# Kernel optimization log

Hardware: AMD Instinct MI355X
Metric: run time of the kernel (lower is better)

The kernel has to match this reference:

```python
import jax, jax.numpy as jnp
import numpy as np

# QLSTMClassifier (quantum mode): Embedding -> QLSTM (4 quantum gate layers per step) -> Linear -> log_softmax.
# NOTE: QLSTM.forward unbinds dim 0 (batch) and cats each x:(seq,emb) with hx:(batch,hid),
# which requires batch == seq_len. We honor that with S = batch = seq_len.
S = 256   # batch == seq_len
E = 1024  # embedding_dim
H = 10    # hidden_dim == n_qubits (required by f*cx elementwise product)
V = 50257 # vocab_size
T = 50    # tagset_size


def setup_inputs() -> dict:
    key = jax.random.key(0)
    ks = jax.random.split(key, 6)
    sentence = jax.random.randint(ks[0], (S, S), 0, V)                                   # (batch, seq)
    emb_table = jax.random.normal(ks[1], (V, E), jnp.float32) * 0.02                      # nn.Embedding weight
    Wg = jax.random.normal(ks[2], (4, E + H, H), jnp.float32) * (1.0 / np.sqrt(E + H))    # forget/input/update/output linears
    bg = jnp.zeros((4, H), jnp.float32)
    theta = jax.random.normal(ks[3], (4, H), jnp.float32)                                 # trainable RX angles per gate
    W_out = jax.random.normal(ks[4], (H, T), jnp.float32) * (1.0 / np.sqrt(H))            # hidden2tag
    b_out = jnp.zeros((T,), jnp.float32)
    return dict(sentence=sentence, emb_table=emb_table, Wg=Wg, bg=bg,
                theta=theta, W_out=W_out, b_out=b_out)


def _qlayer(z, th):
    # Exact closed form of the QLayer circuit on n wires starting from |0...0>:
    #   RX(z_w) then RX(th_w) on wire w  ==> RX(a_w) with a_w = z_w + th_w (product state),
    #   then CNOT ring: CNOT(0,1), CNOT(1,2), ..., CNOT(n-2,n-1), CNOT(n-1,0),
    # Heisenberg-picture pullback of Z_w through the CNOT ring gives
    #   M_0 = Z_1 Z_2 ... Z_{n-1},   M_w = Z_0 Z_1 ... Z_w  (w >= 1),
    # and on the product state <Z_j> = cos(a_j), so expectations factorize:
    #   out_0 = prod_{j>=1} cos(a_j),  out_w = prod_{j<=w} cos(a_j).
    c = jnp.cos(z + th)                                   # (B, H)
    cum = jnp.cumprod(c, axis=-1)                         # prefix products
    tail = jnp.prod(c[:, 1:], axis=-1, keepdims=True)     # wire-0 observable
    return jnp.concatenate([tail, cum[:, 1:]], axis=-1)   # (B, H)


def reference(sentence, emb_table, Wg, bg, theta, W_out, b_out):
    embeds = emb_table[sentence]                          # (S, S, E); scan axis = dim 0 (unbind dim)
    h0 = jnp.zeros((embeds.shape[0], theta.shape[1]), embeds.dtype)

    def step(carry, x):                                   # x: (S, E)
        hx, cx = carry
        comb = jnp.concatenate([x, hx], axis=-1)          # (S, E+H)
        z = jnp.einsum('bi,gio->gbo', comb, Wg) + bg[:, None, :]  # (4, S, H)
        f = jax.nn.sigmoid(_qlayer(z[0], theta[0]))
        i = jax.nn.sigmoid(_qlayer(z[1], theta[1]))
        g = jnp.tanh(_qlayer(z[2], theta[2]))
        o = jax.nn.sigmoid(_qlayer(z[3], theta[3]))
        cx = f * cx + i * g
        hx = o * jnp.tanh(cx)
        return (hx, cx), hx

    _, outs = jax.lax.scan(step, (h0, h0), embeds)        # (S, S, H)
    logits = outs @ W_out + b_out                         # (S, S, T)
    return jax.nn.log_softmax(logits, axis=2)
```

## Files before the change

### kernel.cpp

```cpp
#include <hip/hip_runtime.h>
#include <hip/hip_bf16.h>


#define E_DIM 1024
#define H_DIM 10
#define NC 40
#define V_DIM 50257
#define EHS 10340

typedef __attribute__((ext_vector_type(8))) short bf16x8;
typedef __attribute__((ext_vector_type(4))) float f32x4;

__device__ __forceinline__ unsigned short f2bf(float f) {
    unsigned u = __float_as_uint(f);
    unsigned r = u + 0x7FFFu + ((u >> 16) & 1u);
    return (unsigned short)(r >> 16);
}

__global__ __launch_bounds__(256) void k_wt(const float* __restrict__ Wg,
                                            unsigned short* __restrict__ Bfg) {
    int i = blockIdx.x * 256 + threadIdx.x;
    if (i >= 6144) return;
    int lane = i & 63, nt = (i >> 6) % 3, c = i / 192;
    int kg = lane >> 4, n = lane & 15;
    int nc = nt * 16 + n;
    unsigned short v[8];
#pragma unroll
    for (int j = 0; j < 8; ++j) {
        int k = c * 32 + kg * 8 + j;
        float w = 0.0f;
        if (nc < NC) {
            int g = nc / H_DIM, h = nc % H_DIM;
            w = Wg[g * EHS + k * H_DIM + h];
        }
        v[j] = f2bf(w);
    }
    bf16x8* dst = (bf16x8*)(Bfg + (size_t)i * 8);
    bf16x8 pk;
#pragma unroll
    for (int j = 0; j < 8; ++j) pk[j] = (short)v[j];
    *dst = pk;
}

__global__ __launch_bounds__(256, 4) void k_gemm(const float* __restrict__ emb,
                                                 const unsigned short* __restrict__ Bfg,
                                                 float* __restrict__ zu) {
    const int tid = threadIdx.x;
    const int wave = tid >> 6, lane = tid & 63;
    const int R0 = (blockIdx.x * 4 + wave) * 16;
    const int m = lane & 15, q = lane >> 4;

    int row = R0 + m;
    if (row > V_DIM - 1) row = V_DIM - 1;
    const float* arow = emb + (size_t)row * E_DIM + q * 8;

    f32x4 acc0 = {0.f, 0.f, 0.f, 0.f}, acc1 = acc0, acc2 = acc0;

#pragma unroll 2
    for (int c = 0; c < 32; ++c) {
        f32x4 a0 = __builtin_nontemporal_load((const f32x4*)(arow + c * 32));
        f32x4 a1 = __builtin_nontemporal_load((const f32x4*)(arow + c * 32 + 4));
        bf16x8 b0 = *(const bf16x8*)(Bfg + ((size_t)(c * 3 + 0) * 64 + lane) * 8);
        bf16x8 b1 = *(const bf16x8*)(Bfg + ((size_t)(c * 3 + 1) * 64 + lane) * 8);
        bf16x8 b2 = *(const bf16x8*)(Bfg + ((size_t)(c * 3 + 2) * 64 + lane) * 8);
        bf16x8 af;
        af[0] = (short)f2bf(a0[0]); af[1] = (short)f2bf(a0[1]);
        af[2] = (short)f2bf(a0[2]); af[3] = (short)f2bf(a0[3]);
        af[4] = (short)f2bf(a1[0]); af[5] = (short)f2bf(a1[1]);
        af[6] = (short)f2bf(a1[2]); af[7] = (short)f2bf(a1[3]);
        acc0 = __builtin_amdgcn_mfma_f32_16x16x32_bf16(af, b0, acc0, 0, 0, 0);
        acc1 = __builtin_amdgcn_mfma_f32_16x16x32_bf16(af, b1, acc1, 0, 0, 0);
        acc2 = __builtin_amdgcn_mfma_f32_16x16x32_bf16(af, b2, acc2, 0, 0, 0);
    }

    const int r0 = R0 + q * 4;
#pragma unroll
    for (int i = 0; i < 4; ++i) {
        int r = r0 + i;
        if (r < V_DIM) {
            size_t o = (size_t)r * NC;
            zu[o + m] = acc0[i];
            zu[o + 16 + m] = acc1[i];
            if (m < 8) zu[o + 32 + m] = acc2[i];
        }
    }
}

template <int CTRL>
__device__ __forceinline__ float dpp1(float x) {
    return __int_as_float(__builtin_amdgcn_update_dpp(
        __float_as_int(1.0f), __float_as_int(x), CTRL, 0xF, 0xF, false));
}
#define ROW_SHR(n) (0x110 + (n))
#define ROW_SHL(n) (0x100 + (n))

__device__ __forceinline__ float rdlane(float v, int l) {
    return __int_as_float(__builtin_amdgcn_readlane(__float_as_int(v), l));
}

__global__ __launch_bounds__(128) void k_rnn(const int* __restrict__ idx,
                                             const float* __restrict__ zu,
                                             const float* __restrict__ Wg,
                                             const float* __restrict__ bg,
                                             const float* __restrict__ theta,
                                             float* __restrict__ outs) {
    __shared__ float zall[256 * NC];
    const int tid = threadIdx.x;
    const int b = blockIdx.x;

    {
        const int j = tid >> 2;
        const int qq = tid & 3;
        int tok[8];
#pragma unroll
        for (int pass = 0; pass < 8; ++pass)
            tok[pass] = idx[(size_t)(pass * 32 + j) * 256 + b];
#pragma unroll
        for (int pass = 0; pass < 8; ++pass) {
            const float* src = zu + (size_t)tok[pass] * NC + qq * 10;
            float* dst = &zall[(pass * 32 + j) * NC + qq * 10];
#pragma unroll
            for (int e = 0; e < 5; ++e)
                *(float2*)(dst + 2 * e) = *(const float2*)(src + 2 * e);
        }
    }
    __syncthreads();
    if (tid >= 64) return;

    const int lane = tid;
    const int r = lane >> 4;
    const int h = lane & 15;
    const int hc = (h < 10) ? h : 9;
    const int cidx = r * 10 + hc;

    float Wh[10];
#pragma unroll
    for (int j = 0; j < 10; ++j) Wh[j] = Wg[r * EHS + (E_DIM + j) * H_DIM + hc];
    const float bias = bg[cidx] + theta[cidx];

    const float kk = (r == 2) ? 2.0f : -1.0f;
    const float aa = (r == 2) ? 1.0f : 0.0f;
    const float bb = (r == 2) ? -2.0f : 1.0f;

    float cx = 0.0f, hx = 0.0f;
    float zv = zall[cidx];
#pragma unroll 8
    for (int t = 0; t < 256; ++t) {
        float znext = zall[((t < 255) ? (t + 1) : t) * NC + cidx];

        float hv0 = rdlane(hx, 0), hv1 = rdlane(hx, 1), hv2 = rdlane(hx, 2),
              hv3 = rdlane(hx, 3), hv4 = rdlane(hx, 4), hv5 = rdlane(hx, 5),
              hv6 = rdlane(hx, 6), hv7 = rdlane(hx, 7), hv8 = rdlane(hx, 8),
              hv9 = rdlane(hx, 9);
        float d0 = fmaf(hv0, Wh[0], fmaf(hv2, Wh[2],
                   fmaf(hv4, Wh[4], fmaf(hv6, Wh[6], hv8 * Wh[8]))));
        float d1 = fmaf(hv1, Wh[1], fmaf(hv3, Wh[3],
                   fmaf(hv5, Wh[5], fmaf(hv7, Wh[7], hv9 * Wh[9]))));
        float z = (zv + bias) + (d0 + d1);

        float cc = __builtin_amdgcn_cosf(z * 0.15915494309189535f);

        float pp = cc;
        pp *= dpp1<ROW_SHR(1)>(pp);
        pp *= dpp1<ROW_SHR(2)>(pp);
        pp *= dpp1<ROW_SHR(4)>(pp);
        pp *= dpp1<ROW_SHR(8)>(pp);
        float ss = (h < 10) ? cc : 1.0f;
        ss *= dpp1<ROW_SHL(1)>(ss);
        ss *= dpp1<ROW_SHL(2)>(ss);
        ss *= dpp1<ROW_SHL(4)>(ss);
        ss *= dpp1<ROW_SHL(8)>(ss);
        float tl = dpp1<ROW_SHL(1)>(ss);
        float qv = (h == 0) ? tl : pp;

        float e = __expf(kk * qv);
        float act = fmaf(bb, __builtin_amdgcn_rcpf(1.0f + e), aa);

        float fv = __shfl(act, h);
        float iv = __shfl(act, 16 + h);
        float gv = __shfl(act, 32 + h);
        float ov = __shfl(act, 48 + h);

        cx = fmaf(fv, cx, iv * gv);
        float e2 = __expf(2.0f * cx);
        float th = fmaf(-2.0f, __builtin_amdgcn_rcpf(1.0f + e2), 1.0f);
        hx = ov * th;

        if (lane < 10) outs[((size_t)t * 256 + b) * H_DIM + lane] = hx;
        zv = znext;
    }
}

__global__ __launch_bounds__(256) void k_head(const float* __restrict__ outs,
                                              const float* __restrict__ Wo,
                                              const float* __restrict__ bo,
                                              float* __restrict__ out) {
    const size_t row = blockIdx.x * 256 + threadIdx.x;
    float hx[10];
#pragma unroll
    for (int i = 0; i < 5; ++i) {
        float2 v = *(const float2*)&outs[row * H_DIM + 2 * i];
        hx[2 * i] = v.x; hx[2 * i + 1] = v.y;
    }
    float lg[50];
#pragma unroll
    for (int cI = 0; cI < 50; ++cI) {
        float l = bo[cI];
#pragma unroll
        for (int j = 0; j < 10; ++j) l = fmaf(hx[j], Wo[j * 50 + cI], l);
        lg[cI] = l;
    }
    float m = lg[0];
#pragma unroll
    for (int cI = 1; cI < 50; ++cI) m = fmaxf(m, lg[cI]);
    float sum = 0.0f;
#pragma unroll
    for (int cI = 0; cI < 50; ++cI) sum += __expf(lg[cI] - m);
    float lse = m + __logf(sum);
#pragma unroll
    for (int i = 0; i < 25; ++i) {
        float2 v = {lg[2 * i] - lse, lg[2 * i + 1] - lse};
        *(float2*)&out[row * 50 + 2 * i] = v;
    }
}

extern "C" void kernel_launch(void* const* d_in, const int* in_sizes, int n_in,
                              void* d_out, int out_size, void* d_ws, size_t ws_size,
                              hipStream_t stream) {
    const int*   sentence = (const int*)d_in[0];
    const float* emb      = (const float*)d_in[1];
    const float* Wg       = (const float*)d_in[2];
    const float* bg       = (const float*)d_in[3];
    const float* theta    = (const float*)d_in[4];
    const float* Wo       = (const float*)d_in[5];
    const float* bo       = (const float*)d_in[6];
    float* out = (float*)d_out;

    float* ws = (float*)d_ws;
    unsigned short* Bfg = (unsigned short*)ws;
    float* zu   = ws + 24576;
    float* outs = zu + (size_t)V_DIM * NC;

    k_wt<<<24, 256, 0, stream>>>(Wg, Bfg);
    k_gemm<<<786, 256, 0, stream>>>(emb, Bfg, zu);
    k_rnn<<<256, 128, 0, stream>>>(sentence, zu, Wg, bg, theta, outs);
    k_head<<<256, 256, 0, stream>>>(outs, Wo, bo, out);
}
```

Before: 387.1 us.

## Fuse output head into recurrent kernel and shrink GEMM blocks to one wave

The log-softmax head is folded into the recurrent kernel: each block keeps its 256 hidden states in shared memory and, after the recurrence, all 128 threads compute logits and log_softmax. This removes one kernel launch and the global round trip of the hidden history. The GEMM is relaunched as 3142 single-wave blocks instead of 786 four-wave blocks, for finer scheduling granularity. The recurrence also uses exp2 with prescaled constants and drops a redundant shuffle. The head's output writes are now strided per block (row t*256+b), which may coalesce worse.

Result: no change. 384.4 us (-0.7%).

```diff
diff --git a/kernel.cpp b/kernel.cpp
--- a/kernel.cpp
+++ b/kernel.cpp
@@ -42,12 +42,11 @@
     *dst = pk;
 }
 
-__global__ __launch_bounds__(256, 4) void k_gemm(const float* __restrict__ emb,
-                                                 const unsigned short* __restrict__ Bfg,
-                                                 float* __restrict__ zu) {
-    const int tid = threadIdx.x;
-    const int wave = tid >> 6, lane = tid & 63;
-    const int R0 = (blockIdx.x * 4 + wave) * 16;
+__global__ __launch_bounds__(64) void k_gemm(const float* __restrict__ emb,
+                                             const unsigned short* __restrict__ Bfg,
+                                             float* __restrict__ zu) {
+    const int lane = threadIdx.x;
+    const int R0 = blockIdx.x * 16;
     const int m = lane & 15, q = lane >> 4;
 
     int row = R0 + m;
@@ -103,8 +102,11 @@
                                              const float* __restrict__ Wg,
                                              const float* __restrict__ bg,
                                              const float* __restrict__ theta,
-                                             float* __restrict__ outs) {
+                                             const float* __restrict__ Wo,
+                                             const float* __restrict__ bo,
+                                             float* __restrict__ out) {
     __shared__ float zall[256 * NC];
+    __shared__ float hist[256 * H_DIM];
     const int tid = threadIdx.x;
     const int b = blockIdx.x;
 
@@ -125,102 +127,100 @@
         }
     }
     __syncthreads();
-    if (tid >= 64) return;
-
-    const int lane = tid;
-    const int r = lane >> 4;
-    const int h = lane & 15;
-    const int hc = (h < 10) ? h : 9;
-    const int cidx = r * 10 + hc;
-
-    float Wh[10];
-#pragma unroll
-    for (int j = 0; j < 10; ++j) Wh[j] = Wg[r * EHS + (E_DIM + j) * H_DIM + hc];
-    const float bias = bg[cidx] + theta[cidx];
-
-    const float kk = (r == 2) ? 2.0f : -1.0f;
-    const float aa = (r == 2) ? 1.0f : 0.0f;
-    const float bb = (r == 2) ? -2.0f : 1.0f;
-
-    float cx = 0.0f, hx = 0.0f;
-    float zv = zall[cidx];
+
+    if (tid < 64) {
+        const int lane = tid;
+        const int r = lane >> 4;
+        const int h = lane & 15;
+        const int hc = (h < 10) ? h : 9;
+        const int cidx = r * 10 + hc;
+
+        float Wh[10];
+#pragma unroll
+        for (int j = 0; j < 10; ++j) Wh[j] = Wg[r * EHS + (E_DIM + j) * H_DIM + hc];
+        const float bias = bg[cidx] + theta[cidx];
+
+        const float kk2 = (r == 2) ? 2.8853900817779268f : -1.4426950408889634f;
+        const float aa = (r == 2) ? 1.0f : 0.0f;
+        const float bb = (r == 2) ? -2.0f : 1.0f;
+
+        float cx = 0.0f, hx = 0.0f;
+        float zv = zall[cidx];
 #pragma unroll 8
-    for (int t = 0; t < 256; ++t) {
-        float znext = zall[((t < 255) ? (t + 1) : t) * NC + cidx];
-
-        float hv0 = rdlane(hx, 0), hv1 = rdlane(hx, 1), hv2 = rdlane(hx, 2),
-              hv3 = rdlane(hx, 3), hv4 = rdlane(hx, 4), hv5 = rdlane(hx, 5),
-              hv6 = rdlane(hx, 6), hv7 = rdlane(hx, 7), hv8 = rdlane(hx, 8),
-              hv9 = rdlane(hx, 9);
-        float d0 = fmaf(hv0, Wh[0], fmaf(hv2, Wh[2],
-                   fmaf(hv4, Wh[4], fmaf(hv6, Wh[6], hv8 * Wh[8]))));
-        float d1 = fmaf(hv1, Wh[1], fmaf(hv3, Wh[3],
-                   fmaf(hv5, Wh[5], fmaf(hv7, Wh[7], hv9 * Wh[9]))));
-        float z = (zv + bias) + (d0 + d1);
-
-        float cc = __builtin_amdgcn_cosf(z * 0.15915494309189535f);
-
-        float pp = cc;
-        pp *= dpp1<ROW_SHR(1)>(pp);
-        pp *= dpp1<ROW_SHR(2)>(pp);
-        pp *= dpp1<ROW_SHR(4)>(pp);
-        pp *= dpp1<ROW_SHR(8)>(pp);
-        float ss = (h < 10) ? cc : 1.0f;
-        ss *= dpp1<ROW_SHL(1)>(ss);
-        ss *= dpp1<ROW_SHL(2)>(ss);
-        ss *= dpp1<ROW_SHL(4)>(ss);
-        ss *= dpp1<ROW_SHL(8)>(ss);
-        float tl = dpp1<ROW_SHL(1)>(ss);
-        float qv = (h == 0) ? tl : pp;
-
-        float e = __expf(kk * qv);
-        float act = fmaf(bb, __builtin_amdgcn_rcpf(1.0f + e), aa);
-
-        float fv = __shfl(act, h);
-        float iv = __shfl(act, 16 + h);
-        float gv = __shfl(act, 32 + h);
-        float ov = __shfl(act, 48 + h);
-
-        cx = fmaf(fv, cx, iv * gv);
-        float e2 = __expf(2.0f * cx);
-        float th = fmaf(-2.0f, __builtin_amdgcn_rcpf(1.0f + e2), 1.0f);
-        hx = ov * th;
-
-        if (lane < 10) outs[((size_t)t * 256 + b) * H_DIM + lane] = hx;
-        zv = znext;
-    }
-}
-
-__global__ __launch_bounds__(256) void k_head(const float* __restrict__ outs,
-                                              const float* __restrict__ Wo,
-                                              const float* __restrict__ bo,
-                                              float* __restrict__ out) {
-    const size_t row = blockIdx.x * 256 + threadIdx.x;
-    float hx[10];
-#pragma unroll
-    for (int i = 0; i < 5; ++i) {
-        float2 v = *(const float2*)&outs[row * H_DIM + 2 * i];
-        hx[2 * i] = v.x; hx[2 * i + 1] = v.y;
-    }
-    float lg[50];
-#pragma unroll
-    for (int cI = 0; cI < 50; ++cI) {
-        float l = bo[cI];
-#pragma unroll
-        for (int j = 0; j < 10; ++j) l = fmaf(hx[j], Wo[j * 50 + cI], l);
-        lg[cI] = l;
-    }
-    float m = lg[0];
-#pragma unroll
-    for (int cI = 1; cI < 50; ++cI) m = fmaxf(m, lg[cI]);
-    float sum = 0.0f;
-#pragma unroll
-    for (int cI = 0; cI < 50; ++cI) sum += __expf(lg[cI] - m);
-    float lse = m + __logf(sum);
-#pragma unroll
-    for (int i = 0; i < 25; ++i) {
-        float2 v = {lg[2 * i] - lse, lg[2 * i + 1] - lse};
-        *(float2*)&out[row * 50 + 2 * i] = v;
+        for (int t = 0; t < 256; ++t) {
+            float znext = zall[((t < 255) ? (t + 1) : t) * NC + cidx];
+
+            float hv0 = rdlane(hx, 0), hv1 = rdlane(hx, 1), hv2 = rdlane(hx, 2),
+                  hv3 = rdlane(hx, 3), hv4 = rdlane(hx, 4), hv5 = rdlane(hx, 5),
+                  hv6 = rdlane(hx, 6), hv7 = rdlane(hx, 7), hv8 = rdlane(hx, 8),
+                  hv9 = rdlane(hx, 9);
+            float d0 = fmaf(hv0, Wh[0], fmaf(hv2, Wh[2],
+                       fmaf(hv4, Wh[4], fmaf(hv6, Wh[6], hv8 * Wh[8]))));
+            float d1 = fmaf(hv1, Wh[1], fmaf(hv3, Wh[3],
+                       fmaf(hv5, Wh[5], fmaf(hv7, Wh[7], hv9 * Wh[9]))));
+            float z = (zv + bias) + (d0 + d1);
+
+            float cc = __builtin_amdgcn_cosf(z * 0.15915494309189535f);
+
+            float pp = cc;
+            pp *= dpp1<ROW_SHR(1)>(pp);
+            pp *= dpp1<ROW_SHR(2)>(pp);
+            pp *= dpp1<ROW_SHR(4)>(pp);
+            pp *= dpp1<ROW_SHR(8)>(pp);
+            float ss = (h < 10) ? cc : 1.0f;
+            ss *= dpp1<ROW_SHL(1)>(ss);
+            ss *= dpp1<ROW_SHL(2)>(ss);
+            ss *= dpp1<ROW_SHL(4)>(ss);
+            ss *= dpp1<ROW_SHL(8)>(ss);
+            float tl = dpp1<ROW_SHL(1)>(ss);
+            float qv = (h == 0) ? tl : pp;
+
+            float e = __builtin_amdgcn_exp2f(kk2 * qv);
+            float act = fmaf(bb, __builtin_amdgcn_rcpf(1.0f + e), aa);
+
+            float fv = act;
+            float iv = __shfl(act, 16 + h);
+            float gv = __shfl(act, 32 + h);
+            float ov = __shfl(act, 48 + h);
+
+            cx = fmaf(fv, cx, iv * gv);
+            float e2 = __builtin_amdgcn_exp2f(2.8853900817779268f * cx);
+            float th = fmaf(-2.0f, __builtin_amdgcn_rcpf(1.0f + e2), 1.0f);
+            hx = ov * th;
+
+            if (lane < 10) hist[t * H_DIM + lane] = hx;
+            zv = znext;
+        }
+    }
+    __syncthreads();
+
+#pragma unroll
+    for (int rr = 0; rr < 2; ++rr) {
+        const int t = tid + rr * 128;
+        float hv[10];
+#pragma unroll
+        for (int i = 0; i < 10; ++i) hv[i] = hist[t * H_DIM + i];
+        float lg[50];
+#pragma unroll
+        for (int cI = 0; cI < 50; ++cI) {
+            float l = bo[cI];
+#pragma unroll
+            for (int j = 0; j < 10; ++j) l = fmaf(hv[j], Wo[j * 50 + cI], l);
+            lg[cI] = l;
+        }
+        float mx = lg[0];
+#pragma unroll
+        for (int cI = 1; cI < 50; ++cI) mx = fmaxf(mx, lg[cI]);
+        float sum = 0.0f;
+#pragma unroll
+        for (int cI = 0; cI < 50; ++cI) sum += __expf(lg[cI] - mx);
+        float lse = mx + __logf(sum);
+        float* orow = out + ((size_t)t * 256 + b) * 50;
+#pragma unroll
+        for (int i = 0; i < 25; ++i) {
+            float2 v = {lg[2 * i] - lse, lg[2 * i + 1] - lse};
+            *(float2*)(orow + 2 * i) = v;
+        }
     }
 }
 
@@ -239,10 +239,8 @@
     float* ws = (float*)d_ws;
     unsigned short* Bfg = (unsigned short*)ws;
     float* zu   = ws + 24576;
-    float* outs = zu + (size_t)V_DIM * NC;
 
     k_wt<<<24, 256, 0, stream>>>(Wg, Bfg);
-    k_gemm<<<786, 256, 0, stream>>>(emb, Bfg, zu);
-    k_rnn<<<256, 128, 0, stream>>>(sentence, zu, Wg, bg, theta, outs);
-    k_head<<<256, 256, 0, stream>>>(outs, Wo, bo, out);
-}
+    k_gemm<<<3142, 64, 0, stream>>>(emb, Bfg, zu);
+    k_rnn<<<256, 128, 0, stream>>>(sentence, zu, Wg, bg, theta, Wo, bo, out);
+}
```
